# Kernel tuning notes

Hardware: AMD Instinct MI355X
Metric: run time of the kernel (lower is better)

The kernel has to match this reference:

```python
import jax, jax.numpy as jnp
import numpy as np

B, N, H = 16, 1024, 4
CH = (64, 128, 256, 512)
KV = 960
EPS = 1e-5  # InstanceNorm2d default eps


def setup_inputs() -> dict:
    key = jax.random.key(0)
    ks = jax.random.split(key, 16)
    s = 0.02
    inp = {
        "emb1": jax.random.normal(ks[0], (B, N, CH[0]), jnp.float32),
        "emb2": jax.random.normal(ks[1], (B, N, CH[1]), jnp.float32),
        "emb3": jax.random.normal(ks[2], (B, N, CH[2]), jnp.float32),
        "emb4": jax.random.normal(ks[3], (B, N, CH[3]), jnp.float32),
        "emb_all": jax.random.normal(ks[4], (B, N, KV), jnp.float32),
        # per-head query weights (torch Linear weight layout [out, in])
        "Wq1": jax.random.normal(ks[5], (H, CH[0] // 4, CH[0] // 4), jnp.float32) * s,
        "Wq2": jax.random.normal(ks[6], (H, CH[1] // 4, CH[1] // 4), jnp.float32) * s,
        "Wq3": jax.random.normal(ks[7], (H, CH[2] // 4, CH[2] // 4), jnp.float32) * s,
        "Wq4": jax.random.normal(ks[8], (H, CH[3] // 4, CH[3] // 4), jnp.float32) * s,
        # NOTE: original forward only ever uses self.key[0] / self.value[0]
        "Wk": jax.random.normal(ks[9], (KV // 4, KV // 4), jnp.float32) * s,
        "Wv": jax.random.normal(ks[10], (KV // 4, KV // 4), jnp.float32) * s,
        "Wo1": jax.random.normal(ks[11], (CH[0], CH[0]), jnp.float32) * s,
        "Wo2": jax.random.normal(ks[12], (CH[1], CH[1]), jnp.float32) * s,
        "Wo3": jax.random.normal(ks[13], (CH[2], CH[2]), jnp.float32) * s,
        "Wo4": jax.random.normal(ks[14], (CH[3], CH[3]), jnp.float32) * s,
    }
    return inp


def _heads_from_all(x):
    # Reproduce the per-head channel regrouping of emb_all:
    # head h takes [16h:16(h+1)] of scale1, [32h:...] of scale2, etc. -> [B,H,N,240]
    b, n, _ = x.shape
    parts = [
        x[:, :, 0:64].reshape(b, n, H, 16),
        x[:, :, 64:192].reshape(b, n, H, 32),
        x[:, :, 192:448].reshape(b, n, H, 64),
        x[:, :, 448:960].reshape(b, n, H, 128),
    ]
    return jnp.concatenate(parts, axis=-1).transpose(0, 2, 1, 3)


def _scale_attn(emb, Wq, Wo, Kh, Vh):
    b, n, c = emb.shape
    d = c // H
    q = emb.reshape(b, n, H, d)
    # per-head linear (torch: x @ W.T): [B,H,N,d]
    Qh = jnp.einsum('bnhd,hed->bhne', q, Wq)
    # channel attention: Q^T K -> [B,H,d,240]
    scores = jnp.einsum('bhnd,bhnk->bhdk', Qh, Kh) / np.float32(np.sqrt(KV))
    # InstanceNorm2d over heads (per (b,h), normalize over last two dims, biased var)
    m = scores.mean(axis=(2, 3), keepdims=True)
    v = scores.var(axis=(2, 3), keepdims=True)
    probs = jax.nn.softmax((scores - m) / jnp.sqrt(v + EPS), axis=-1)
    # probs @ V^T -> [B,H,d,N]
    ctx = jnp.einsum('bhdk,bhnk->bhdn', probs, Vh)
    # permute(0,3,2,1) -> [B,N,d,H], flatten -> [B,N,c]
    ctx = ctx.transpose(0, 3, 2, 1).reshape(b, n, c)
    return jnp.einsum('bnc,ec->bne', ctx, Wo)


def reference(emb1, emb2, emb3, emb4, emb_all,
              Wq1, Wq2, Wq3, Wq4, Wk, Wv, Wo1, Wo2, Wo3, Wo4):
    heads = _heads_from_all(emb_all)  # [B,H,N,240]
    Kh = jnp.einsum('bhnd,ed->bhne', heads, Wk)
    Vh = jnp.einsum('bhnd,ed->bhne', heads, Wv)
    O1 = _scale_attn(emb1, Wq1, Wo1, Kh, Vh)
    O2 = _scale_attn(emb2, Wq2, Wo2, Kh, Vh)
    O3 = _scale_attn(emb3, Wq3, Wo3, Kh, Vh)
    O4 = _scale_attn(emb4, Wq4, Wo4, Kh, Vh)
    return (O1, O2, O3, O4)
```

## Files before the change

### kernel.cpp

```cpp
#include <hip/hip_runtime.h>
#include <hip/hip_bf16.h>
#include <math.h>

#define B_   16
#define N_   1024
#define H_   4
#define D240 240
#define SC_  57600

typedef unsigned short ushort;
typedef __attribute__((ext_vector_type(8))) short bf16x8;
typedef __attribute__((ext_vector_type(8))) unsigned short u16x8;
typedef __attribute__((ext_vector_type(4))) float f32x4;

__device__ __forceinline__ ushort f2b(float v) {
  __hip_bfloat16 h = __float2bfloat16(v);
  return *reinterpret_cast<ushort*>(&h);
}

__device__ __forceinline__ void gload16(const void* g, void* s) {
  __builtin_amdgcn_global_load_lds((const __attribute__((address_space(1))) void*)g,
                                   (__attribute__((address_space(3))) void*)s, 16, 0, 0);
}

#define CI_R 4
__global__ __launch_bounds__(256) void conv_inputs(const float* __restrict__ emb_all,
                                                   const float* __restrict__ e1,
                                                   const float* __restrict__ e2,
                                                   const float* __restrict__ e3,
                                                   const float* __restrict__ e4,
                                                   ushort* __restrict__ heads,
                                                   ushort* __restrict__ embh) {
  __shared__ __align__(16) float lds[CI_R * 960];
  const int t = threadIdx.x;
  const int bx = blockIdx.x;
  const int which = bx >> 12;
  const int bn0 = (bx & 4095) * CI_R;

  if (which == 0) {
    const float4* src = (const float4*)(emb_all + (long)bn0 * 960);
    float4* dst = (float4*)lds;
    #pragma unroll
    for (int j = 0; j < 4; ++j) {
      int idx = j * 256 + t;
      if (idx < 960) dst[idx] = src[idx];
    }
  } else {
    #pragma unroll
    for (int j = 0; j < 4; ++j) {
      int idx = j * 256 + t;
      if (idx < 960) {
        const float* sp; int i, c, sbase;
        if (idx < 64)       { i = idx >> 4;          c = idx & 15;   sp = e1 + ((long)(bn0 + i)) * 64  + c * 4; sbase = 0;   }
        else if (idx < 192) { int r = idx - 64;  i = r >> 5; c = r & 31;  sp = e2 + ((long)(bn0 + i)) * 128 + c * 4; sbase = 64;  }
        else if (idx < 448) { int r = idx - 192; i = r >> 6; c = r & 63;  sp = e3 + ((long)(bn0 + i)) * 256 + c * 4; sbase = 192; }
        else                { int r = idx - 448; i = r >> 7; c = r & 127; sp = e4 + ((long)(bn0 + i)) * 512 + c * 4; sbase = 448; }
        *(float4*)(lds + i * 960 + sbase + c * 4) = *(const float4*)sp;
      }
    }
  }
  __syncthreads();

  ushort* dbase = which ? embh : heads;
  #pragma unroll
  for (int jj = 0; jj < 2; ++jj) {
    const int cidx = jj * 256 + t;
    const int g = cidx & 31, q = cidx >> 5;
    const int h = q & 3, i = q >> 2;
    const int k0 = g * 8;
    const int bn = bn0 + i;
    const int b = bn >> 10, n = bn & 1023;
    u16x8 w;
    if (k0 < 240) {
      int soff;
      if (k0 < 16)       soff = h * 16 + k0;
      else if (k0 < 48)  soff = 64  + h * 32  + (k0 - 16);
      else if (k0 < 112) soff = 192 + h * 64  + (k0 - 48);
      else               soff = 448 + h * 128 + (k0 - 112);
      const float* s = lds + i * 960 + soff;
      float4 p0 = *(const float4*)s;
      float4 p1 = *(const float4*)(s + 4);
      w[0] = f2b(p0.x); w[1] = f2b(p0.y); w[2] = f2b(p0.z); w[3] = f2b(p0.w);
      w[4] = f2b(p1.x); w[5] = f2b(p1.y); w[6] = f2b(p1.z); w[7] = f2b(p1.w);
    } else {
      w = (u16x8)0;
    }
    *(u16x8*)(dbase + (((long)b * H_ + h) * N_ + n) * 256 + k0) = w;
  }
}

__global__ __launch_bounds__(256) void conv_weights(
    const float* __restrict__ Wk, const float* __restrict__ Wv,
    const float* __restrict__ q1, const float* __restrict__ q2,
    const float* __restrict__ q3, const float* __restrict__ q4,
    const float* __restrict__ o1, const float* __restrict__ o2,
    const float* __restrict__ o3, const float* __restrict__ o4,
    ushort* __restrict__ wts) {
  long i = (long)blockIdx.x * 256 + threadIdx.x;
  if (i >= 716800) return;
  float v = 0.f;
  if (i < 122880) {
    const float* src = (i < 61440) ? Wk : Wv;
    long j = (i < 61440) ? i : i - 61440;
    int r = j / 256, k = j % 256;
    if (k < 240) v = src[(long)r * 240 + k];
  } else if (i < 368640) {
    long j = i - 122880;
    int h = j / 61440; int rem = j % 61440;
    int r = rem / 256, k = rem % 256;
    int s = r < 16 ? 0 : r < 48 ? 1 : r < 112 ? 2 : 3;
    const int dss[4] = {16, 32, 64, 128};
    const int qf[4]  = {0, 16, 48, 112};
    const float* qs[4] = {q1, q2, q3, q4};
    int d = dss[s], off = qf[s];
    if (k >= off && k < off + d)
      v = qs[s][((long)(h * d + (r - off))) * d + (k - off)];
  } else {
    long j = i - 368640;
    int s = j < 4096 ? 0 : j < 20480 ? 1 : j < 86016 ? 2 : 3;
    const long base[4] = {0, 4096, 20480, 86016};
    const int cs[4] = {64, 128, 256, 512};
    const float* os[4] = {o1, o2, o3, o4};
    long rem = j - base[s];
    int c = cs[s], d = c >> 2;
    int e = rem / c, kk = rem % c;
    v = os[s][(long)e * c + (kk % d) * 4 + kk / d];
  }
  wts[i] = f2b(v);
}

__device__ __forceinline__ void gemm_core_b16(
    ushort* As, ushort* Bs,
    const ushort* __restrict__ A, long lda,
    const ushort* __restrict__ Bm, long ldb,
    ushort* __restrict__ C, long ldc,
    int M, int Nn, int Npad, int K, int m0, int n0)
{
  const int tid = threadIdx.x;
  const int l = tid & 63, w = tid >> 6;
  const int wy = w >> 1, wx = w & 1;

  f32x4 acc[4][4];
  #pragma unroll
  for (int i = 0; i < 4; ++i)
    #pragma unroll
    for (int j = 0; j < 4; ++j) acc[i][j] = (f32x4)0.f;

  const int srow = tid >> 2;
  const int skc  = (tid & 3) * 8;
  int ra0 = m0 + srow;      ra0 = ra0 < M  ? ra0 : M - 1;
  int ra1 = m0 + srow + 64; ra1 = ra1 < M  ? ra1 : M - 1;
  int rb0 = n0 + srow;      rb0 = rb0 < Nn ? rb0 : Nn - 1;
  int rb1 = n0 + srow + 64; rb1 = rb1 < Nn ? rb1 : Nn - 1;
  const ushort* a0 = A  + (long)ra0 * lda + skc;
  const ushort* a1 = A  + (long)ra1 * lda + skc;
  const ushort* b0 = Bm + (long)rb0 * ldb + skc;
  const ushort* b1 = Bm + (long)rb1 * ldb + skc;
  ushort* lA0 = As + srow * 32 + skc;
  ushort* lA1 = As + (srow + 64) * 32 + skc;
  ushort* lB0 = Bs + srow * 32 + skc;
  ushort* lB1 = Bs + (srow + 64) * 32 + skc;

  const ushort* arp = As + (wy * 64 + (l & 15)) * 32 + (l >> 4) * 8;
  const ushort* brp = Bs + (wx * 64 + (l & 15)) * 32 + (l >> 4) * 8;

  for (int k0 = 0; k0 < K; k0 += 32) {
    __syncthreads();
    gload16(a0 + k0, lA0);
    gload16(a1 + k0, lA1);
    gload16(b0 + k0, lB0);
    gload16(b1 + k0, lB1);
    __syncthreads();
    bf16x8 af[4], bfr[4];
    #pragma unroll
    for (int i = 0; i < 4; ++i) af[i]  = *(const bf16x8*)(arp + i * 512);
    #pragma unroll
    for (int j = 0; j < 4; ++j) bfr[j] = *(const bf16x8*)(brp + j * 512);
    #pragma unroll
    for (int i = 0; i < 4; ++i)
      #pragma unroll
      for (int j = 0; j < 4; ++j)
        acc[i][j] = __builtin_amdgcn_mfma_f32_16x16x32_bf16(af[i], bfr[j], acc[i][j], 0, 0, 0);
  }

  const int quad = l >> 4, lc = l & 15;
  #pragma unroll
  for (int i = 0; i < 4; ++i) {
    #pragma unroll
    for (int r = 0; r < 4; ++r) {
      int row = m0 + wy * 64 + i * 16 + quad * 4 + r;
      if (row >= M) continue;
      ushort* Cr = C + (long)row * ldc;
      #pragma unroll
      for (int j = 0; j < 4; ++j) {
        int col = n0 + wx * 64 + j * 16 + lc;
        if (col < Nn) Cr[col] = f2b(acc[i][j][r]);
        else if (col < Npad) Cr[col] = 0;
      }
    }
  }
}

__global__ __launch_bounds__(256) void mfma_proj(
    const ushort* __restrict__ heads_b, const ushort* __restrict__ emb_h,
    const ushort* __restrict__ Wk_b, const ushort* __restrict__ Wv_b,
    const ushort* __restrict__ Wq_bd,
    ushort* __restrict__ Kh_T, ushort* __restrict__ Vh, ushort* __restrict__ Q_T)
{
  __shared__ __align__(16) ushort As[128 * 32];
  __shared__ __align__(16) ushort Bs[128 * 32];
  const int bx = blockIdx.x;
  const long sbh = 1024L * 256;

  if (bx < 1024) {
    const int bh = bx >> 4, t = bx & 15;
    gemm_core_b16(As, Bs,
                  Wk_b, 256,
                  heads_b + (long)bh * sbh, 256,
                  Kh_T + (long)bh * 240 * 1024, 1024,
                  240, 1024, 1024, 256, (t >> 3) * 128, (t & 7) * 128);
  } else if (bx < 2048) {
    const int local = bx - 1024;
    const int bh = local >> 4, t = local & 15;
    gemm_core_b16(As, Bs,
                  heads_b + (long)bh * sbh, 256,
                  Wv_b, 256,
                  Vh + (long)bh * sbh, 256,
                  1024, 240, 256, 256, (t >> 1) * 128, (t & 1) * 128);
  } else {
    const int local = bx - 2048;
    const int bh = local >> 4, t = local & 15;
    const int h = bh & 3;
    gemm_core_b16(As, Bs,
                  Wq_bd + h * 61440, 256,
                  emb_h + (long)bh * sbh, 256,
                  Q_T + (long)bh * 240 * 1024, 1024,
                  240, 1024, 1024, 256, (t >> 3) * 128, (t & 7) * 128);
  }
}

__global__ __launch_bounds__(256) void mfma_abT(
    const ushort* __restrict__ A, long lda, long AsY, long AsZ,
    const ushort* __restrict__ Bm, long ldb, long BsY, long BsZ,
    void* __restrict__ Cv, long ldc, long CsY, long CsZ,
    int M, int Nn, int Npad, int K, float alpha, int c_bf16, int tilesN)
{
  A  += blockIdx.y * AsY + blockIdx.z * AsZ;
  Bm += blockIdx.y * BsY + blockIdx.z * BsZ;

  const int m0 = (blockIdx.x / tilesN) * 128;
  const int n0 = (blockIdx.x % tilesN) * 128;
  const int tid = threadIdx.x;
  const int l = tid & 63, w = tid >> 6;
  const int wy = w >> 1, wx = w & 1;

  __shared__ __align__(16) ushort As[128 * 32];
  __shared__ __align__(16) ushort Bs[128 * 32];

  f32x4 acc[4][4];
  #pragma unroll
  for (int i = 0; i < 4; ++i)
    #pragma unroll
    for (int j = 0; j < 4; ++j) acc[i][j] = (f32x4)0.f;

  const int srow = tid >> 2;
  const int skc  = (tid & 3) * 8;
  int ra0 = m0 + srow;      ra0 = ra0 < M  ? ra0 : M - 1;
  int ra1 = m0 + srow + 64; ra1 = ra1 < M  ? ra1 : M - 1;
  int rb0 = n0 + srow;      rb0 = rb0 < Nn ? rb0 : Nn - 1;
  int rb1 = n0 + srow + 64; rb1 = rb1 < Nn ? rb1 : Nn - 1;
  const ushort* a0 = A  + (long)ra0 * lda + skc;
  const ushort* a1 = A  + (long)ra1 * lda + skc;
  const ushort* b0 = Bm + (long)rb0 * ldb + skc;
  const ushort* b1 = Bm + (long)rb1 * ldb + skc;
  ushort* lA0 = As + srow * 32 + skc;
  ushort* lA1 = As + (srow + 64) * 32 + skc;
  ushort* lB0 = Bs + srow * 32 + skc;
  ushort* lB1 = Bs + (srow + 64) * 32 + skc;

  const ushort* arp = As + (wy * 64 + (l & 15)) * 32 + (l >> 4) * 8;
  const ushort* brp = Bs + (wx * 64 + (l & 15)) * 32 + (l >> 4) * 8;

  for (int k0 = 0; k0 < K; k0 += 32) {
    __syncthreads();
    gload16(a0 + k0, lA0);
    gload16(a1 + k0, lA1);
    gload16(b0 + k0, lB0);
    gload16(b1 + k0, lB1);
    __syncthreads();
    bf16x8 af[4], bfr[4];
    #pragma unroll
    for (int i = 0; i < 4; ++i) af[i]  = *(const bf16x8*)(arp + i * 512);
    #pragma unroll
    for (int j = 0; j < 4; ++j) bfr[j] = *(const bf16x8*)(brp + j * 512);
    #pragma unroll
    for (int i = 0; i < 4; ++i)
      #pragma unroll
      for (int j = 0; j < 4; ++j)
        acc[i][j] = __builtin_amdgcn_mfma_f32_16x16x32_bf16(af[i], bfr[j], acc[i][j], 0, 0, 0);
  }

  const int quad = l >> 4, lc = l & 15;
  if (c_bf16) {
    ushort* C = (ushort*)Cv + blockIdx.y * CsY + blockIdx.z * CsZ;
    #pragma unroll
    for (int i = 0; i < 4; ++i) {
      #pragma unroll
      for (int r = 0; r < 4; ++r) {
        int row = m0 + wy * 64 + i * 16 + quad * 4 + r;
        if (row >= M) continue;
        ushort* Cr = C + (long)row * ldc;
        #pragma unroll
        for (int j = 0; j < 4; ++j) {
          int col = n0 + wx * 64 + j * 16 + lc;
          if (col < Nn) Cr[col] = f2b(acc[i][j][r] * alpha);
          else if (col < Npad) Cr[col] = 0;
        }
      }
    }
  } else {
    float* C = (float*)Cv + blockIdx.y * CsY + blockIdx.z * CsZ;
    #pragma unroll
    for (int i = 0; i < 4; ++i) {
      #pragma unroll
      for (int r = 0; r < 4; ++r) {
        int row = m0 + wy * 64 + i * 16 + quad * 4 + r;
        if (row >= M) continue;
        float* Cr = C + (long)row * ldc;
        #pragma unroll
        for (int j = 0; j < 4; ++j) {
          int col = n0 + wx * 64 + j * 16 + lc;
          if (col < Nn) Cr[col] = acc[i][j][r] * alpha;
        }
      }
    }
  }
}

__global__ __launch_bounds__(256) void mfma_ctx(const ushort* __restrict__ V,
                                                const ushort* __restrict__ P,
                                                ushort* __restrict__ ctx2) {
  const int h = blockIdx.y, b = blockIdx.z;
  const ushort* A  = V + (((long)b * H_ + h) * 1024) * 256;
  const ushort* Bm = P + (((long)b * H_ + h) * 240) * 256;

  const int m0 = (blockIdx.x >> 1) * 128;
  const int n0 = (blockIdx.x & 1) * 128;
  const int tid = threadIdx.x;
  const int l = tid & 63, w = tid >> 6;
  const int wy = w >> 1, wx = w & 1;

  __shared__ __align__(16) ushort As[128 * 32];
  __shared__ __align__(16) ushort Bs[128 * 32];

  f32x4 acc[4][4];
  #pragma unroll
  for (int i = 0; i < 4; ++i)
    #pragma unroll
    for (int j = 0; j < 4; ++j) acc[i][j] = (f32x4)0.f;

  const int srow = tid >> 2;
  const int skc  = (tid & 3) * 8;
  int rb0 = n0 + srow;      rb0 = rb0 < 240 ? rb0 : 239;
  int rb1 = n0 + srow + 64; rb1 = rb1 < 240 ? rb1 : 239;
  const ushort* a0 = A  + (long)(m0 + srow) * 256 + skc;
  const ushort* a1 = A  + (long)(m0 + srow + 64) * 256 + skc;
  const ushort* b0 = Bm + (long)rb0 * 256 + skc;
  const ushort* b1 = Bm + (long)rb1 * 256 + skc;
  ushort* lA0 = As + srow * 32 + skc;
  ushort* lA1 = As + (srow + 64) * 32 + skc;
  ushort* lB0 = Bs + srow * 32 + skc;
  ushort* lB1 = Bs + (srow + 64) * 32 + skc;

  const ushort* arp = As + (wy * 64 + (l & 15)) * 32 + (l >> 4) * 8;
  const ushort* brp = Bs + (wx * 64 + (l & 15)) * 32 + (l >> 4) * 8;

  for (int k0 = 0; k0 < 256; k0 += 32) {
    __syncthreads();
    gload16(a0 + k0, lA0);
    gload16(a1 + k0, lA1);
    gload16(b0 + k0, lB0);
    gload16(b1 + k0, lB1);
    __syncthreads();
    bf16x8 af[4], bfr[4];
    #pragma unroll
    for (int i = 0; i < 4; ++i) af[i]  = *(const bf16x8*)(arp + i * 512);
    #pragma unroll
    for (int j = 0; j < 4; ++j) bfr[j] = *(const bf16x8*)(brp + j * 512);
    #pragma unroll
    for (int i = 0; i < 4; ++i)
      #pragma unroll
      for (int j = 0; j < 4; ++j)
        acc[i][j] = __builtin_amdgcn_mfma_f32_16x16x32_bf16(af[i], bfr[j], acc[i][j], 0, 0, 0);
  }

  const int quad = l >> 4, lc = l & 15;
  const int dss[4] = {16, 32, 64, 128};
  const int qf[4]  = {0, 16, 48, 112};
  const int cf[4]  = {0, 64, 192, 448};
  #pragma unroll
  for (int i = 0; i < 4; ++i) {
    #pragma unroll
    for (int r = 0; r < 4; ++r) {
      int row = m0 + wy * 64 + i * 16 + quad * 4 + r;
      ushort* Cr = ctx2 + ((long)b * N_ + row) * 960;
      #pragma unroll
      for (int j = 0; j < 4; ++j) {
        int col = n0 + wx * 64 + j * 16 + lc;
        if (col < 240) {
          int s = col < 16 ? 0 : col < 48 ? 1 : col < 112 ? 2 : 3;
          int chan = cf[s] + h * dss[s] + (col - qf[s]);
          Cr[chan] = f2b(acc[i][j][r]);
        }
      }
    }
  }
}

__global__ __launch_bounds__(256) void mfma_oproj(const ushort* __restrict__ ctx2,
                                                  const ushort* __restrict__ Wo_b,
                                                  float* __restrict__ out) {
  const int bx = blockIdx.x;
  int s = bx < 128 ? 0 : bx < 256 ? 1 : bx < 512 ? 2 : 3;
  const int sbase[4] = {0, 128, 256, 512};
  const int cs_[4]   = {64, 128, 256, 512};
  const int coff_[4] = {0, 64, 192, 448};
  const int wo_[4]   = {0, 4096, 20480, 86016};
  const long oo_[4]  = {0, 1048576, 3145728, 7340032};
  const int c = cs_[s];
  const int nt = (c + 127) >> 7;
  const int local = bx - sbase[s];
  const int m0 = (local / nt) * 128;
  const int n0 = (local % nt) * 128;

  const ushort* A  = ctx2 + coff_[s];
  const ushort* Bm = Wo_b + wo_[s];
  float* C = out + oo_[s];
  const int K = c, Nn = c;

  const int tid = threadIdx.x;
  const int l = tid & 63, w = tid >> 6;
  const int wy = w >> 1, wx = w & 1;

  __shared__ __align__(16) ushort As[128 * 32];
  __shared__ __align__(16) ushort Bs[128 * 32];

  f32x4 acc[4][4];
  #pragma unroll
  for (int i = 0; i < 4; ++i)
    #pragma unroll
    for (int j = 0; j < 4; ++j) acc[i][j] = (f32x4)0.f;

  const int srow = tid >> 2;
  const int skc  = (tid & 3) * 8;
  int rb0 = n0 + srow;      rb0 = rb0 < Nn ? rb0 : Nn - 1;
  int rb1 = n0 + srow + 64; rb1 = rb1 < Nn ? rb1 : Nn - 1;
  const ushort* a0 = A  + (long)(m0 + srow) * 960 + skc;
  const ushort* a1 = A  + (long)(m0 + srow + 64) * 960 + skc;
  const ushort* b0 = Bm + (long)rb0 * c + skc;
  const ushort* b1 = Bm + (long)rb1 * c + skc;
  ushort* lA0 = As + srow * 32 + skc;
  ushort* lA1 = As + (srow + 64) * 32 + skc;
  ushort* lB0 = Bs + srow * 32 + skc;
  ushort* lB1 = Bs + (srow + 64) * 32 + skc;

  const ushort* arp = As + (wy * 64 + (l & 15)) * 32 + (l >> 4) * 8;
  const ushort* brp = Bs + (wx * 64 + (l & 15)) * 32 + (l >> 4) * 8;

  for (int k0 = 0; k0 < K; k0 += 32) {
    __syncthreads();
    gload16(a0 + k0, lA0);
    gload16(a1 + k0, lA1);
    gload16(b0 + k0, lB0);
    gload16(b1 + k0, lB1);
    __syncthreads();
    bf16x8 af[4], bfr[4];
    #pragma unroll
    for (int i = 0; i < 4; ++i) af[i]  = *(const bf16x8*)(arp + i * 512);
    #pragma unroll
    for (int j = 0; j < 4; ++j) bfr[j] = *(const bf16x8*)(brp + j * 512);
    #pragma unroll
    for (int i = 0; i < 4; ++i)
      #pragma unroll
      for (int j = 0; j < 4; ++j)
        acc[i][j] = __builtin_amdgcn_mfma_f32_16x16x32_bf16(af[i], bfr[j], acc[i][j], 0, 0, 0);
  }

  const int quad = l >> 4, lc = l & 15;
  #pragma unroll
  for (int i = 0; i < 4; ++i) {
    #pragma unroll
    for (int r = 0; r < 4; ++r) {
      int row = m0 + wy * 64 + i * 16 + quad * 4 + r;
      float* Cr = C + (long)row * c;
      #pragma unroll
      for (int j = 0; j < 4; ++j) {
        int col = n0 + wx * 64 + j * 16 + lc;
        if (col < Nn) Cr[col] = acc[i][j][r];
      }
    }
  }
}

__global__ __launch_bounds__(256) void in_stats(const float* __restrict__ sc0,
                                                const float* __restrict__ sc1,
                                                float* __restrict__ stats) {
  const int doffs[4] = {0, 16, 48, 112};
  const int dss[4]   = {16, 32, 64, 128};
  const int bh = blockIdx.x, sidx = blockIdx.y;
  const long base = (long)bh * SC_ + doffs[sidx] * D240;
  const float4* A4 = (const float4*)(sc0 + base);
  const float4* B4 = (const float4*)(sc1 + base);
  const int n4 = dss[sidx] * 60;

  float s = 0.f, s2 = 0.f;
  for (int i = threadIdx.x; i < n4; i += 256) {
    float4 a = A4[i], b = B4[i];
    float x0 = a.x + b.x, x1 = a.y + b.y, x2 = a.z + b.z, x3 = a.w + b.w;
    s  += x0 + x1 + x2 + x3;
    s2 += x0 * x0 + x1 * x1 + x2 * x2 + x3 * x3;
  }
  #pragma unroll
  for (int o = 32; o > 0; o >>= 1) { s += __shfl_down(s, o); s2 += __shfl_down(s2, o); }

  __shared__ float wsum[4], wsum2[4];
  const int wave = threadIdx.x >> 6, lane = threadIdx.x & 63;
  if (lane == 0) { wsum[wave] = s; wsum2[wave] = s2; }
  __syncthreads();
  if (threadIdx.x == 0) {
    float n = (float)(n4 * 4);
    float ts = wsum[0] + wsum[1] + wsum[2] + wsum[3];
    float ts2 = wsum2[0] + wsum2[1] + wsum2[2] + wsum2[3];
    float mean = ts / n;
    float var = ts2 / n - mean * mean;
    stats[(bh * 4 + sidx) * 2]     = mean;
    stats[(bh * 4 + sidx) * 2 + 1] = rsqrtf(var + 1e-5f);
  }
}

__global__ __launch_bounds__(256) void sm_apply(const float* __restrict__ sc0,
                                                const float* __restrict__ sc1,
                                                const float* __restrict__ stats,
                                                ushort* __restrict__ P) {
  const int bh = blockIdx.y;
  const int row = blockIdx.x * 4 + (threadIdx.x >> 6);
  const int lane = threadIdx.x & 63;
  const int s = row < 16 ? 0 : row < 48 ? 1 : row < 112 ? 2 : 3;
  const float mean = stats[(bh * 4 + s) * 2];
  const float rstd = stats[(bh * 4 + s) * 2 + 1];
  const long base = (long)bh * SC_ + (long)row * D240;
  const float* r0 = sc0 + base;
  const float* r1 = sc1 + base;
  ushort* p = P + ((long)bh * D240 + row) * 256;

  float v[4];
  float mx = -1e30f;
  #pragma unroll
  for (int j = 0; j < 4; ++j) {
    int c = lane + j * 64;
    v[j] = (c < D240) ? (r0[c] + r1[c] - mean) * rstd : -1e30f;
    mx = fmaxf(mx, v[j]);
  }
  #pragma unroll
  for (int o = 32; o > 0; o >>= 1) mx = fmaxf(mx, __shfl_xor(mx, o));
  float sum = 0.f;
  #pragma unroll
  for (int j = 0; j < 4; ++j) {
    int c = lane + j * 64;
    v[j] = (c < D240) ? __expf(v[j] - mx) : 0.f;
    sum += v[j];
  }
  #pragma unroll
  for (int o = 32; o > 0; o >>= 1) sum += __shfl_xor(sum, o);
  float inv = 1.f / sum;
  #pragma unroll
  for (int j = 0; j < 4; ++j) {
    int c = lane + j * 64;
    p[c] = (c < D240) ? f2b(v[j] * inv) : (ushort)0;
  }
}

extern "C" void kernel_launch(void* const* d_in, const int* in_sizes, int n_in,
                              void* d_out, int out_size, void* d_ws, size_t ws_size,
                              hipStream_t stream) {
  const float* emb[4] = {(const float*)d_in[0], (const float*)d_in[1],
                         (const float*)d_in[2], (const float*)d_in[3]};
  const float* emb_all = (const float*)d_in[4];
  const float* Wq[4] = {(const float*)d_in[5], (const float*)d_in[6],
                        (const float*)d_in[7], (const float*)d_in[8]};
  const float* Wk = (const float*)d_in[9];
  const float* Wv = (const float*)d_in[10];
  const float* Wo[4] = {(const float*)d_in[11], (const float*)d_in[12],
                        (const float*)d_in[13], (const float*)d_in[14]};
  float* out = (float*)d_out;
  float* sc0 = (float*)d_out;
  float* sc1 = (float*)d_out + 64L * SC_;

  ushort* wsb     = (ushort*)d_ws;
  ushort* heads_b = wsb;
  ushort* ctx2    = wsb;
  ushort* emb_h   = wsb + 16777216;
  ushort* P_b     = wsb + 16777216;
  ushort* Q_T     = wsb + 33554432;
  ushort* Kh_T    = wsb + 49283072;
  ushort* Vh      = wsb + 65011712;
  ushort* wts     = wsb + 81788928;
  ushort* Wk_b  = wts;
  ushort* Wv_b  = wts + 61440;
  ushort* Wq_bd = wts + 122880;
  ushort* Wo_b  = wts + 368640;
  float*  stats = (float*)(wsb + 82505728);

  const float alpha_s = 1.0f / sqrtf(960.0f);

  conv_inputs<<<dim3(8192), 256, 0, stream>>>(emb_all, emb[0], emb[1], emb[2], emb[3],
                                              heads_b, emb_h);
  conv_weights<<<dim3(2800), 256, 0, stream>>>(Wk, Wv, Wq[0], Wq[1], Wq[2], Wq[3],
                                               Wo[0], Wo[1], Wo[2], Wo[3], wts);

  mfma_proj<<<dim3(3072), 256, 0, stream>>>(heads_b, emb_h, Wk_b, Wv_b, Wq_bd,
                                            Kh_T, Vh, Q_T);

  mfma_abT<<<dim3(4, 64, 2), 256, 0, stream>>>(
      Q_T, 1024, 240L * 1024, 512,
      Kh_T, 1024, 240L * 1024, 512,
      sc0, 240, (long)SC_, 64L * SC_,
      240, 240, 240, 512, alpha_s, 0, 2);

  in_stats<<<dim3(64, 4), 256, 0, stream>>>(sc0, sc1, stats);
  sm_apply<<<dim3(60, 64), 256, 0, stream>>>(sc0, sc1, stats, P_b);

  mfma_ctx<<<dim3(16, H_, B_), 256, 0, stream>>>(Vh, P_b, ctx2);

  mfma_oproj<<<dim3(1024), 256, 0, stream>>>(ctx2, Wo_b, out);
}
```

Baseline: 344.4 us.

## Fuse fp32-to-bf16 input regrouping into projection GEMM tile loads

```diff
diff --git a/kernel.cpp b/kernel.cpp
--- a/kernel.cpp
+++ b/kernel.cpp
@@ -18,75 +18,37 @@
   return *reinterpret_cast<ushort*>(&h);
 }
 
+__device__ __forceinline__ u16x8 cvt8(float4 a, float4 b) {
+  u16x8 w;
+  w[0] = f2b(a.x); w[1] = f2b(a.y); w[2] = f2b(a.z); w[3] = f2b(a.w);
+  w[4] = f2b(b.x); w[5] = f2b(b.y); w[6] = f2b(b.z); w[7] = f2b(b.w);
+  return w;
+}
+
 __device__ __forceinline__ void gload16(const void* g, void* s) {
   __builtin_amdgcn_global_load_lds((const __attribute__((address_space(1))) void*)g,
                                    (__attribute__((address_space(3))) void*)s, 16, 0, 0);
 }
 
-#define CI_R 4
-__global__ __launch_bounds__(256) void conv_inputs(const float* __restrict__ emb_all,
-                                                   const float* __restrict__ e1,
-                                                   const float* __restrict__ e2,
-                                                   const float* __restrict__ e3,
-                                                   const float* __restrict__ e4,
-                                                   ushort* __restrict__ heads,
-                                                   ushort* __restrict__ embh) {
-  __shared__ __align__(16) float lds[CI_R * 960];
-  const int t = threadIdx.x;
-  const int bx = blockIdx.x;
-  const int which = bx >> 12;
-  const int bn0 = (bx & 4095) * CI_R;
-
-  if (which == 0) {
-    const float4* src = (const float4*)(emb_all + (long)bn0 * 960);
-    float4* dst = (float4*)lds;
-    #pragma unroll
-    for (int j = 0; j < 4; ++j) {
-      int idx = j * 256 + t;
-      if (idx < 960) dst[idx] = src[idx];
-    }
-  } else {
-    #pragma unroll
-    for (int j = 0; j < 4; ++j) {
-      int idx = j * 256 + t;
-      if (idx < 960) {
-        const float* sp; int i, c, sbase;
-        if (idx < 64)       { i = idx >> 4;          c = idx & 15;   sp = e1 + ((long)(bn0 + i)) * 64  + c * 4; sbase = 0;   }
-        else if (idx < 192) { int r = idx - 64;  i = r >> 5; c = r & 31;  sp = e2 + ((long)(bn0 + i)) * 128 + c * 4; sbase = 64;  }
-        else if (idx < 448) { int r = idx - 192; i = r >> 6; c = r & 63;  sp = e3 + ((long)(bn0 + i)) * 256 + c * 4; sbase = 192; }
-        else                { int r = idx - 448; i = r >> 7; c = r & 127; sp = e4 + ((long)(bn0 + i)) * 512 + c * 4; sbase = 448; }
-        *(float4*)(lds + i * 960 + sbase + c * 4) = *(const float4*)sp;
-      }
-    }
-  }
-  __syncthreads();
-
-  ushort* dbase = which ? embh : heads;
-  #pragma unroll
-  for (int jj = 0; jj < 2; ++jj) {
-    const int cidx = jj * 256 + t;
-    const int g = cidx & 31, q = cidx >> 5;
-    const int h = q & 3, i = q >> 2;
-    const int k0 = g * 8;
-    const int bn = bn0 + i;
-    const int b = bn >> 10, n = bn & 1023;
-    u16x8 w;
-    if (k0 < 240) {
-      int soff;
-      if (k0 < 16)       soff = h * 16 + k0;
-      else if (k0 < 48)  soff = 64  + h * 32  + (k0 - 16);
-      else if (k0 < 112) soff = 192 + h * 64  + (k0 - 48);
-      else               soff = 448 + h * 128 + (k0 - 112);
-      const float* s = lds + i * 960 + soff;
-      float4 p0 = *(const float4*)s;
-      float4 p1 = *(const float4*)(s + 4);
-      w[0] = f2b(p0.x); w[1] = f2b(p0.y); w[2] = f2b(p0.z); w[3] = f2b(p0.w);
-      w[4] = f2b(p1.x); w[5] = f2b(p1.y); w[6] = f2b(p1.z); w[7] = f2b(p1.w);
-    } else {
-      w = (u16x8)0;
-    }
-    *(u16x8*)(dbase + (((long)b * H_ + h) * N_ + n) * 256 + k0) = w;
-  }
+__device__ __forceinline__ const float* heads_src(const float* __restrict__ emb_all,
+                                                  int b, int n, int h, int k) {
+  int soff;
+  if (k < 16)       soff = h * 16 + k;
+  else if (k < 48)  soff = 64  + h * 32  + (k - 16);
+  else if (k < 112) soff = 192 + h * 64  + (k - 48);
+  else              soff = 448 + h * 128 + (k - 112);
+  return emb_all + ((long)b * N_ + n) * 960 + soff;
+}
+
+__device__ __forceinline__ const float* emb_src(const float* __restrict__ e1,
+                                                const float* __restrict__ e2,
+                                                const float* __restrict__ e3,
+                                                const float* __restrict__ e4,
+                                                int b, int n, int h, int k, int* stride) {
+  if (k < 16)  { *stride = 64;  return e1 + ((long)b * N_ + n) * 64  + h * 16  + k; }
+  if (k < 48)  { *stride = 128; return e2 + ((long)b * N_ + n) * 128 + h * 32  + (k - 16); }
+  if (k < 112) { *stride = 256; return e3 + ((long)b * N_ + n) * 256 + h * 64  + (k - 48); }
+  *stride = 512; return e4 + ((long)b * N_ + n) * 512 + h * 128 + (k - 112);
 }
 
 __global__ __launch_bounds__(256) void conv_weights(
@@ -129,12 +91,14 @@
   wts[i] = f2b(v);
 }
 
-__device__ __forceinline__ void gemm_core_b16(
+__device__ __forceinline__ void core_w_g(
     ushort* As, ushort* Bs,
-    const ushort* __restrict__ A, long lda,
-    const ushort* __restrict__ Bm, long ldb,
-    ushort* __restrict__ C, long ldc,
-    int M, int Nn, int Npad, int K, int m0, int n0)
+    const ushort* __restrict__ Aw, long lda, int M,
+    const float* __restrict__ emb_all,
+    const float* __restrict__ e1, const float* __restrict__ e2,
+    const float* __restrict__ e3, const float* __restrict__ e4,
+    int gmode, int b, int h,
+    ushort* __restrict__ C, long ldc, int m0, int n0, int K)
 {
   const int tid = threadIdx.x;
   const int l = tid & 63, w = tid >> 6;
@@ -148,18 +112,15 @@
 
   const int srow = tid >> 2;
   const int skc  = (tid & 3) * 8;
-  int ra0 = m0 + srow;      ra0 = ra0 < M  ? ra0 : M - 1;
-  int ra1 = m0 + srow + 64; ra1 = ra1 < M  ? ra1 : M - 1;
-  int rb0 = n0 + srow;      rb0 = rb0 < Nn ? rb0 : Nn - 1;
-  int rb1 = n0 + srow + 64; rb1 = rb1 < Nn ? rb1 : Nn - 1;
-  const ushort* a0 = A  + (long)ra0 * lda + skc;
-  const ushort* a1 = A  + (long)ra1 * lda + skc;
-  const ushort* b0 = Bm + (long)rb0 * ldb + skc;
-  const ushort* b1 = Bm + (long)rb1 * ldb + skc;
+  int ra0 = m0 + srow;      ra0 = ra0 < M ? ra0 : M - 1;
+  int ra1 = m0 + srow + 64; ra1 = ra1 < M ? ra1 : M - 1;
+  const ushort* a0 = Aw + (long)ra0 * lda + skc;
+  const ushort* a1 = Aw + (long)ra1 * lda + skc;
   ushort* lA0 = As + srow * 32 + skc;
   ushort* lA1 = As + (srow + 64) * 32 + skc;
   ushort* lB0 = Bs + srow * 32 + skc;
   ushort* lB1 = Bs + (srow + 64) * 32 + skc;
+  const int nrow = n0 + srow;
 
   const ushort* arp = As + (wy * 64 + (l & 15)) * 32 + (l >> 4) * 8;
   const ushort* brp = Bs + (wx * 64 + (l & 15)) * 32 + (l >> 4) * 8;
@@ -168,8 +129,21 @@
     __syncthreads();
     gload16(a0 + k0, lA0);
     gload16(a1 + k0, lA1);
-    gload16(b0 + k0, lB0);
-    gload16(b1 + k0, lB1);
+    const int k = k0 + skc;
+    u16x8 w0, w1;
+    if (k < 240) {
+      const float* s0; int stride;
+      if (gmode == 0) { stride = 960; s0 = heads_src(emb_all, b, nrow, h, k); }
+      else            { s0 = emb_src(e1, e2, e3, e4, b, nrow, h, k, &stride); }
+      const float* s1 = s0 + (long)64 * stride;
+      float4 p0 = *(const float4*)s0, p1 = *(const float4*)(s0 + 4);
+      float4 q0 = *(const float4*)s1, q1 = *(const float4*)(s1 + 4);
+      w0 = cvt8(p0, p1); w1 = cvt8(q0, q1);
+    } else {
+      w0 = (u16x8)0; w1 = (u16x8)0;
+    }
+    *(u16x8*)lB0 = w0;
+    *(u16x8*)lB1 = w1;
     __syncthreads();
     bf16x8 af[4], bfr[4];
     #pragma unroll
@@ -190,6 +164,83 @@
     for (int r = 0; r < 4; ++r) {
       int row = m0 + wy * 64 + i * 16 + quad * 4 + r;
       if (row >= M) continue;
+      ushort* Cr = C + (long)row * ldc;
+      #pragma unroll
+      for (int j = 0; j < 4; ++j) {
+        int col = n0 + wx * 64 + j * 16 + lc;
+        Cr[col] = f2b(acc[i][j][r]);
+      }
+    }
+  }
+}
+
+__device__ __forceinline__ void core_g_w(
+    ushort* As, ushort* Bs,
+    const float* __restrict__ emb_all, int b, int h,
+    const ushort* __restrict__ Bw, long ldb, int Nn, int Npad,
+    ushort* __restrict__ C, long ldc, int m0, int n0, int K)
+{
+  const int tid = threadIdx.x;
+  const int l = tid & 63, w = tid >> 6;
+  const int wy = w >> 1, wx = w & 1;
+
+  f32x4 acc[4][4];
+  #pragma unroll
+  for (int i = 0; i < 4; ++i)
+    #pragma unroll
+    for (int j = 0; j < 4; ++j) acc[i][j] = (f32x4)0.f;
+
+  const int srow = tid >> 2;
+  const int skc  = (tid & 3) * 8;
+  int rb0 = n0 + srow;      rb0 = rb0 < Nn ? rb0 : Nn - 1;
+  int rb1 = n0 + srow + 64; rb1 = rb1 < Nn ? rb1 : Nn - 1;
+  const ushort* b0 = Bw + (long)rb0 * ldb + skc;
+  const ushort* b1 = Bw + (long)rb1 * ldb + skc;
+  ushort* lA0 = As + srow * 32 + skc;
+  ushort* lA1 = As + (srow + 64) * 32 + skc;
+  ushort* lB0 = Bs + srow * 32 + skc;
+  ushort* lB1 = Bs + (srow + 64) * 32 + skc;
+  const int mrow = m0 + srow;
+
+  const ushort* arp = As + (wy * 64 + (l & 15)) * 32 + (l >> 4) * 8;
+  const ushort* brp = Bs + (wx * 64 + (l & 15)) * 32 + (l >> 4) * 8;
+
+  for (int k0 = 0; k0 < K; k0 += 32) {
+    __syncthreads();
+    gload16(b0 + k0, lB0);
+    gload16(b1 + k0, lB1);
+    const int k = k0 + skc;
+    u16x8 w0, w1;
+    if (k < 240) {
+      const float* s0 = heads_src(emb_all, b, mrow, h, k);
+      const float* s1 = s0 + (long)64 * 960;
+      float4 p0 = *(const float4*)s0, p1 = *(const float4*)(s0 + 4);
+      float4 q0 = *(const float4*)s1, q1 = *(const float4*)(s1 + 4);
+      w0 = cvt8(p0, p1); w1 = cvt8(q0, q1);
+    } else {
+      w0 = (u16x8)0; w1 = (u16x8)0;
+    }
+    *(u16x8*)lA0 = w0;
+    *(u16x8*)lA1 = w1;
+    __syncthreads();
+    bf16x8 af[4], bfr[4];
+    #pragma unroll
+    for (int i = 0; i < 4; ++i) af[i]  = *(const bf16x8*)(arp + i * 512);
+    #pragma unroll
+    for (int j = 0; j < 4; ++j) bfr[j] = *(const bf16x8*)(brp + j * 512);
+    #pragma unroll
+    for (int i = 0; i < 4; ++i)
+      #pragma unroll
+      for (int j = 0; j < 4; ++j)
+        acc[i][j] = __builtin_amdgcn_mfma_f32_16x16x32_bf16(af[i], bfr[j], acc[i][j], 0, 0, 0);
+  }
+
+  const int quad = l >> 4, lc = l & 15;
+  #pragma unroll
+  for (int i = 0; i < 4; ++i) {
+    #pragma unroll
+    for (int r = 0; r < 4; ++r) {
+      int row = m0 + wy * 64 + i * 16 + quad * 4 + r;
       ushort* Cr = C + (long)row * ldc;
       #pragma unroll
       for (int j = 0; j < 4; ++j) {
@@ -202,7 +253,9 @@
 }
 
 __global__ __launch_bounds__(256) void mfma_proj(
-    const ushort* __restrict__ heads_b, const ushort* __restrict__ emb_h,
+    const float* __restrict__ emb_all,
+    const float* __restrict__ e1, const float* __restrict__ e2,
+    const float* __restrict__ e3, const float* __restrict__ e4,
     const ushort* __restrict__ Wk_b, const ushort* __restrict__ Wv_b,
     const ushort* __restrict__ Wq_bd,
     ushort* __restrict__ Kh_T, ushort* __restrict__ Vh, ushort* __restrict__ Q_T)
@@ -210,32 +263,30 @@
   __shared__ __align__(16) ushort As[128 * 32];
   __shared__ __align__(16) ushort Bs[128 * 32];
   const int bx = blockIdx.x;
-  const long sbh = 1024L * 256;
 
   if (bx < 1024) {
     const int bh = bx >> 4, t = bx & 15;
-    gemm_core_b16(As, Bs,
-                  Wk_b, 256,
-                  heads_b + (long)bh * sbh, 256,
-                  Kh_T + (long)bh * 240 * 1024, 1024,
-                  240, 1024, 1024, 256, (t >> 3) * 128, (t & 7) * 128);
+    const int b = bh >> 2, h = bh & 3;
+    core_w_g(As, Bs, Wk_b, 256, 240,
+             emb_all, e1, e2, e3, e4, 0, b, h,
+             Kh_T + (long)bh * 240 * 1024, 1024,
+             (t >> 3) * 128, (t & 7) * 128, 256);
   } else if (bx < 2048) {
     const int local = bx - 1024;
     const int bh = local >> 4, t = local & 15;
-    gemm_core_b16(As, Bs,
-                  heads_b + (long)bh * sbh, 256,
-                  Wv_b, 256,
-                  Vh + (long)bh * sbh, 256,
-                  1024, 240, 256, 256, (t >> 1) * 128, (t & 1) * 128);
+    const int b = bh >> 2, h = bh & 3;
+    core_g_w(As, Bs, emb_all, b, h,
+             Wv_b, 256, 240, 256,
+             Vh + (long)bh * 1024 * 256, 256,
+             (t >> 1) * 128, (t & 1) * 128, 256);
   } else {
     const int local = bx - 2048;
     const int bh = local >> 4, t = local & 15;
-    const int h = bh & 3;
-    gemm_core_b16(As, Bs,
-                  Wq_bd + h * 61440, 256,
-                  emb_h + (long)bh * sbh, 256,
-                  Q_T + (long)bh * 240 * 1024, 1024,
-                  240, 1024, 1024, 256, (t >> 3) * 128, (t & 7) * 128);
+    const int b = bh >> 2, h = bh & 3;
+    core_w_g(As, Bs, Wq_bd + h * 61440, 256, 240,
+             emb_all, e1, e2, e3, e4, 1, b, h,
+             Q_T + (long)bh * 240 * 1024, 1024,
+             (t >> 3) * 128, (t & 7) * 128, 256);
   }
 }
 
@@ -597,9 +648,7 @@
   float* sc1 = (float*)d_out + 64L * SC_;
 
   ushort* wsb     = (ushort*)d_ws;
-  ushort* heads_b = wsb;
   ushort* ctx2    = wsb;
-  ushort* emb_h   = wsb + 16777216;
   ushort* P_b     = wsb + 16777216;
   ushort* Q_T     = wsb + 33554432;
   ushort* Kh_T    = wsb + 49283072;
@@ -613,13 +662,11 @@
 
   const float alpha_s = 1.0f / sqrtf(960.0f);
 
-  conv_inputs<<<dim3(8192), 256, 0, stream>>>(emb_all, emb[0], emb[1], emb[2], emb[3],
-                                              heads_b, emb_h);
   conv_weights<<<dim3(2800), 256, 0, stream>>>(Wk, Wv, Wq[0], Wq[1], Wq[2], Wq[3],
                                                Wo[0], Wo[1], Wo[2], Wo[3], wts);
 
-  mfma_proj<<<dim3(3072), 256, 0, stream>>>(heads_b, emb_h, Wk_b, Wv_b, Wq_bd,
-                                            Kh_T, Vh, Q_T);
+  mfma_proj<<<dim3(3072), 256, 0, stream>>>(emb_all, emb[0], emb[1], emb[2], emb[3],
+                                            Wk_b, Wv_b, Wq_bd, Kh_T, Vh, Q_T);
 
   mfma_abT<<<dim3(4, 64, 2), 256, 0, stream>>>(
       Q_T, 1024, 240L * 1024, 512,
```

New measurement: 350.4 us. Within noise of the previous version (+1.7%).
